# Performance work log

Hardware: AMD Instinct MI355X
Metric: run time of the kernel (lower is better)

## Reference

```python
import jax, jax.numpy as jnp
import numpy as np


def setup_inputs() -> dict:
    key = jax.random.key(0)
    k1, k2, k3 = jax.random.split(key, 3)
    B, S, I, H, M = 8, 2048, 256, 256, 1024
    x = jax.random.normal(k1, (B, S, I), dtype=jnp.float32)
    mem = jax.random.normal(k2, (B, M, H), dtype=jnp.float32)
    # Xavier-uniform with gain=sqrt(2): bound = sqrt(2)*sqrt(6/(H+I))
    bound = np.sqrt(2.0) * np.sqrt(6.0 / (H + I))
    W = jax.random.uniform(k3, (H, I), dtype=jnp.float32, minval=-bound, maxval=bound)
    return {"x": x, "mem": mem, "W": W}


def reference(x, mem, W):
    # key[b,s,h] = relu(sum_i x[b,s,i] * W[h,i])  -- one batched GEMM for all t
    key_seq = jax.nn.relu(jnp.einsum("bsi,hi->bsh", x, W))
    # val[b,s,m] = sum_h key[b,s,h] * mem[b,m,h]
    val_seq = jnp.einsum("bsh,bmh->bsm", key_seq, mem)
    return key_seq, val_seq
```

## Files before the change

### kernel.cpp

```cpp
#include <hip/hip_runtime.h>
#include <hip/hip_bf16.h>
#include <cstdint>

typedef unsigned short u16;
typedef __bf16 bf16x8 __attribute__((ext_vector_type(8)));
typedef float f32x4 __attribute__((ext_vector_type(4)));
typedef u16 u16x8 __attribute__((ext_vector_type(8)));

#define NX 4194304L

__device__ __forceinline__ u16 f2bf(float f) {
  union { float f; uint32_t u; } v; v.f = f;
  uint32_t r = v.u + 0x7fffu + ((v.u >> 16) & 1u);
  return (u16)(r >> 16);
}

__device__ __forceinline__ u16x8 cvt8(float4 a, float4 b) {
  u16x8 o;
  o[0]=f2bf(a.x); o[1]=f2bf(a.y); o[2]=f2bf(a.z); o[3]=f2bf(a.w);
  o[4]=f2bf(b.x); o[5]=f2bf(b.y); o[6]=f2bf(b.z); o[7]=f2bf(b.w);
  return o;
}

template<bool A_BF16, bool RELU, bool STORE_BF16>
__global__ __launch_bounds__(256, 2)
void gemm_fused(const void* __restrict__ Ap, const float* __restrict__ Bp,
                float* __restrict__ C, u16* __restrict__ Cbf,
                int N, int K,
                long sA_batch, long sB_batch, long sC_batch)
{
  __shared__ __align__(16) u16 sA[128 * 32];
  __shared__ __align__(16) u16 sB[128 * 32];
  const int tid  = threadIdx.x;
  const int wave = tid >> 6;
  const int lane = tid & 63;
  const int quad = lane >> 4;
  const int r    = lane & 15;
  const int wm   = wave >> 1;
  const int wn   = wave & 1;
  const int bm   = blockIdx.y * 128;
  const int bn   = blockIdx.x * 128;
  const int batch = blockIdx.z;

  const int rowL = tid >> 1;
  const int colL = (tid & 1) * 16;

  const float* Bg = Bp + (long)batch * sB_batch + (long)(bn + rowL) * K + colL;
  const float* Af = nullptr;
  const u16*   Ah = nullptr;
  if (A_BF16) Ah = (const u16*)Ap + (long)batch * sA_batch + (long)(bm + rowL) * K + colL;
  else        Af = (const float*)Ap + (long)batch * sA_batch + (long)(bm + rowL) * K + colL;

  u16* dA = sA + rowL * 32 + colL;
  u16* dB = sB + rowL * 32 + colL;

  f32x4 acc[4][4];
  #pragma unroll
  for (int i = 0; i < 4; i++)
    #pragma unroll
    for (int j = 0; j < 4; j++)
      acc[i][j] = f32x4{0.f, 0.f, 0.f, 0.f};

  float4 ra[4], rb[4];
  uint4  ha[2];

  if (A_BF16) {
    ha[0] = *(const uint4*)(Ah);
    ha[1] = *(const uint4*)(Ah + 8);
  } else {
    ra[0] = *(const float4*)(Af);
    ra[1] = *(const float4*)(Af + 4);
    ra[2] = *(const float4*)(Af + 8);
    ra[3] = *(const float4*)(Af + 12);
  }
  rb[0] = *(const float4*)(Bg);
  rb[1] = *(const float4*)(Bg + 4);
  rb[2] = *(const float4*)(Bg + 8);
  rb[3] = *(const float4*)(Bg + 12);

  for (int kt = 0; kt < K; kt += 32) {
    __syncthreads();
    if (A_BF16) {
      *(uint4*)dA       = ha[0];
      *(uint4*)(dA + 8) = ha[1];
    } else {
      *(u16x8*)dA       = cvt8(ra[0], ra[1]);
      *(u16x8*)(dA + 8) = cvt8(ra[2], ra[3]);
    }
    *(u16x8*)dB       = cvt8(rb[0], rb[1]);
    *(u16x8*)(dB + 8) = cvt8(rb[2], rb[3]);
    __syncthreads();

    const int kn = kt + 32;
    if (kn < K) {
      if (A_BF16) {
        ha[0] = *(const uint4*)(Ah + kn);
        ha[1] = *(const uint4*)(Ah + kn + 8);
      } else {
        ra[0] = *(const float4*)(Af + kn);
        ra[1] = *(const float4*)(Af + kn + 4);
        ra[2] = *(const float4*)(Af + kn + 8);
        ra[3] = *(const float4*)(Af + kn + 12);
      }
      rb[0] = *(const float4*)(Bg + kn);
      rb[1] = *(const float4*)(Bg + kn + 4);
      rb[2] = *(const float4*)(Bg + kn + 8);
      rb[3] = *(const float4*)(Bg + kn + 12);
    }

    bf16x8 af[4], bf[4];
    #pragma unroll
    for (int i = 0; i < 4; i++)
      af[i] = *(const bf16x8*)(sA + (wm * 64 + i * 16 + r) * 32 + quad * 8);
    #pragma unroll
    for (int j = 0; j < 4; j++)
      bf[j] = *(const bf16x8*)(sB + (wn * 64 + j * 16 + r) * 32 + quad * 8);
    #pragma unroll
    for (int i = 0; i < 4; i++)
      #pragma unroll
      for (int j = 0; j < 4; j++)
        acc[i][j] = __builtin_amdgcn_mfma_f32_16x16x32_bf16(af[i], bf[j], acc[i][j], 0, 0, 0);
  }

  float* Co = C + (long)batch * sC_batch;
  u16*   Bo = STORE_BF16 ? (Cbf + (long)batch * sC_batch) : nullptr;
  #pragma unroll
  for (int i = 0; i < 4; i++) {
    #pragma unroll
    for (int j = 0; j < 4; j++) {
      #pragma unroll
      for (int reg = 0; reg < 4; reg++) {
        const int row = bm + wm * 64 + i * 16 + quad * 4 + reg;
        const int col = bn + wn * 64 + j * 16 + r;
        float v = acc[i][j][reg];
        if (RELU) v = v > 0.f ? v : 0.f;
        const long idx = (long)row * N + col;
        Co[idx] = v;
        if (STORE_BF16) Bo[idx] = f2bf(v);
      }
    }
  }
}

extern "C" void kernel_launch(void* const* d_in, const int* in_sizes, int n_in,
                              void* d_out, int out_size, void* d_ws, size_t ws_size,
                              hipStream_t stream) {
  const float* x   = (const float*)d_in[0];
  const float* mem = (const float*)d_in[1];
  const float* W   = (const float*)d_in[2];
  float* out   = (float*)d_out;
  float* key_f = out;
  float* val_f = out + NX;
  u16* key_bf  = (u16*)d_ws;

  dim3 g1(2, 128, 1);
  gemm_fused<false, true, true><<<g1, 256, 0, stream>>>(
      (const void*)x, W, key_f, key_bf, 256, 256, 0, 0, 0);

  dim3 g2(8, 16, 8);
  gemm_fused<true, false, false><<<g2, 256, 0, stream>>>(
      (const void*)key_bf, mem, val_f, nullptr, 1024, 256,
      (long)2048 * 256, (long)1024 * 256, (long)2048 * 1024);
}
```

Before: 149.6 us.

## Stage full-K B tile in swizzled LDS and load A fragments directly from global

```diff
diff --git a/kernel.cpp b/kernel.cpp
--- a/kernel.cpp
+++ b/kernel.cpp
@@ -1,5 +1,4 @@
 #include <hip/hip_runtime.h>
-#include <hip/hip_bf16.h>
 #include <cstdint>
 
 typedef unsigned short u16;
@@ -22,15 +21,19 @@
   return o;
 }
 
+__device__ __forceinline__ int sw_addr(int row, int k) {
+  return row * 256 + ((((k >> 3) ^ (row & 7)) << 3)) + (k & 7);
+}
+
 template<bool A_BF16, bool RELU, bool STORE_BF16>
 __global__ __launch_bounds__(256, 2)
-void gemm_fused(const void* __restrict__ Ap, const float* __restrict__ Bp,
-                float* __restrict__ C, u16* __restrict__ Cbf,
-                int N, int K,
-                long sA_batch, long sB_batch, long sC_batch)
+void gemm_direct(const void* __restrict__ Ap, const float* __restrict__ Bp,
+                 float* __restrict__ C, u16* __restrict__ Cbf, int N,
+                 long sA_batch, long sB_batch, long sC_batch)
 {
-  __shared__ __align__(16) u16 sA[128 * 32];
-  __shared__ __align__(16) u16 sB[128 * 32];
+  constexpr int K = 256;
+  __shared__ __align__(16) u16 sB[128 * 256];
+
   const int tid  = threadIdx.x;
   const int wave = tid >> 6;
   const int lane = tid & 63;
@@ -42,17 +45,30 @@
   const int bn   = blockIdx.x * 128;
   const int batch = blockIdx.z;
 
-  const int rowL = tid >> 1;
-  const int colL = (tid & 1) * 16;
+  {
+    const int rowS = tid >> 1;
+    const int colS = (tid & 1) * 16;
+    const float* Bg = Bp + (long)batch * sB_batch + (long)(bn + rowS) * K + colS;
+    #pragma unroll
+    for (int c = 0; c < 8; ++c) {
+      const float* p = Bg + c * 32;
+      float4 f0 = *(const float4*)(p);
+      float4 f1 = *(const float4*)(p + 4);
+      float4 f2 = *(const float4*)(p + 8);
+      float4 f3 = *(const float4*)(p + 12);
+      u16x8 lo = cvt8(f0, f1);
+      u16x8 hi = cvt8(f2, f3);
+      const int col = colS + c * 32;
+      *(u16x8*)(sB + sw_addr(rowS, col))     = lo;
+      *(u16x8*)(sB + sw_addr(rowS, col + 8)) = hi;
+    }
+  }
+  __syncthreads();
 
-  const float* Bg = Bp + (long)batch * sB_batch + (long)(bn + rowL) * K + colL;
   const float* Af = nullptr;
   const u16*   Ah = nullptr;
-  if (A_BF16) Ah = (const u16*)Ap + (long)batch * sA_batch + (long)(bm + rowL) * K + colL;
-  else        Af = (const float*)Ap + (long)batch * sA_batch + (long)(bm + rowL) * K + colL;
-
-  u16* dA = sA + rowL * 32 + colL;
-  u16* dB = sB + rowL * 32 + colL;
+  if (A_BF16) Ah = (const u16*)Ap   + (long)batch * sA_batch + (long)(bm + wm * 64 + r) * K;
+  else        Af = (const float*)Ap + (long)batch * sA_batch + (long)(bm + wm * 64 + r) * K;
 
   f32x4 acc[4][4];
   #pragma unroll
@@ -61,64 +77,28 @@
     for (int j = 0; j < 4; j++)
       acc[i][j] = f32x4{0.f, 0.f, 0.f, 0.f};
 
-  float4 ra[4], rb[4];
-  uint4  ha[2];
-
-  if (A_BF16) {
-    ha[0] = *(const uint4*)(Ah);
-    ha[1] = *(const uint4*)(Ah + 8);
-  } else {
-    ra[0] = *(const float4*)(Af);
-    ra[1] = *(const float4*)(Af + 4);
-    ra[2] = *(const float4*)(Af + 8);
-    ra[3] = *(const float4*)(Af + 12);
-  }
-  rb[0] = *(const float4*)(Bg);
-  rb[1] = *(const float4*)(Bg + 4);
-  rb[2] = *(const float4*)(Bg + 8);
-  rb[3] = *(const float4*)(Bg + 12);
-
+  #pragma unroll 2
   for (int kt = 0; kt < K; kt += 32) {
-    __syncthreads();
-    if (A_BF16) {
-      *(uint4*)dA       = ha[0];
-      *(uint4*)(dA + 8) = ha[1];
-    } else {
-      *(u16x8*)dA       = cvt8(ra[0], ra[1]);
-      *(u16x8*)(dA + 8) = cvt8(ra[2], ra[3]);
-    }
-    *(u16x8*)dB       = cvt8(rb[0], rb[1]);
-    *(u16x8*)(dB + 8) = cvt8(rb[2], rb[3]);
-    __syncthreads();
-
-    const int kn = kt + 32;
-    if (kn < K) {
-      if (A_BF16) {
-        ha[0] = *(const uint4*)(Ah + kn);
-        ha[1] = *(const uint4*)(Ah + kn + 8);
-      } else {
-        ra[0] = *(const float4*)(Af + kn);
-        ra[1] = *(const float4*)(Af + kn + 4);
-        ra[2] = *(const float4*)(Af + kn + 8);
-        ra[3] = *(const float4*)(Af + kn + 12);
-      }
-      rb[0] = *(const float4*)(Bg + kn);
-      rb[1] = *(const float4*)(Bg + kn + 4);
-      rb[2] = *(const float4*)(Bg + kn + 8);
-      rb[3] = *(const float4*)(Bg + kn + 12);
-    }
-
     bf16x8 af[4], bf[4];
     #pragma unroll
-    for (int i = 0; i < 4; i++)
-      af[i] = *(const bf16x8*)(sA + (wm * 64 + i * 16 + r) * 32 + quad * 8);
+    for (int i = 0; i < 4; ++i) {
+      if (A_BF16) {
+        af[i] = *(const bf16x8*)(Ah + (long)i * 16 * K + kt + quad * 8);
+      } else {
+        const float* p = Af + (long)i * 16 * K + kt + quad * 8;
+        float4 a0 = *(const float4*)(p);
+        float4 a1 = *(const float4*)(p + 4);
+        u16x8 t = cvt8(a0, a1);
+        af[i] = *(bf16x8*)&t;
+      }
+    }
     #pragma unroll
-    for (int j = 0; j < 4; j++)
-      bf[j] = *(const bf16x8*)(sB + (wn * 64 + j * 16 + r) * 32 + quad * 8);
+    for (int j = 0; j < 4; ++j)
+      bf[j] = *(const bf16x8*)(sB + sw_addr(wn * 64 + j * 16 + r, kt + quad * 8));
     #pragma unroll
-    for (int i = 0; i < 4; i++)
+    for (int i = 0; i < 4; ++i)
       #pragma unroll
-      for (int j = 0; j < 4; j++)
+      for (int j = 0; j < 4; ++j)
         acc[i][j] = __builtin_amdgcn_mfma_f32_16x16x32_bf16(af[i], bf[j], acc[i][j], 0, 0, 0);
   }
 
@@ -154,11 +134,11 @@
   u16* key_bf  = (u16*)d_ws;
 
   dim3 g1(2, 128, 1);
-  gemm_fused<false, true, true><<<g1, 256, 0, stream>>>(
-      (const void*)x, W, key_f, key_bf, 256, 256, 0, 0, 0);
+  gemm_direct<false, true, true><<<g1, 256, 0, stream>>>(
+      (const void*)x, W, key_f, key_bf, 256, 0, 0, 0);
 
   dim3 g2(8, 16, 8);
-  gemm_fused<true, false, false><<<g2, 256, 0, stream>>>(
-      (const void*)key_bf, mem, val_f, nullptr, 1024, 256,
+  gemm_direct<true, false, false><<<g2, 256, 0, stream>>>(
+      (const void*)key_bf, mem, val_f, nullptr, 1024,
       (long)2048 * 256, (long)1024 * 256, (long)2048 * 1024);
 }
```

Result: faster. 138.5 us (-7.4%).
